# Optimization experiments

Hardware: AMD Instinct MI355X
Metric: run time of the kernel (lower is better)

Reference implementation:

```python
import jax, jax.numpy as jnp
import numpy as np

NUM_PAGES = 1024
PAGE_SIZE = 64
KV_HEADS = 8
HEAD_DIM = 128
NUM_TOKENS = 8192


def setup_inputs() -> dict:
    key = jax.random.key(0)
    k1, k2, k3 = jax.random.split(key, 3)
    kv_pages = jnp.zeros((NUM_PAGES, PAGE_SIZE, 2 * KV_HEADS, HEAD_DIM), dtype=jnp.float32)
    new_k = jax.random.normal(k1, (NUM_TOKENS, KV_HEADS, HEAD_DIM), dtype=jnp.float32)
    new_v = jax.random.normal(k2, (NUM_TOKENS, KV_HEADS, HEAD_DIM), dtype=jnp.float32)
    # distinct random destination slots (irregular but deterministic scatter);
    # mark a small tail as padding (-1) to exercise the drop path.
    dests = jax.random.permutation(k3, NUM_PAGES * PAGE_SIZE)[:NUM_TOKENS].astype(jnp.int32)
    pad = jnp.arange(NUM_TOKENS) >= (NUM_TOKENS - 128)
    token_dests = jnp.where(pad, jnp.int32(-1), dests)
    return {"kv_pages": kv_pages, "new_k": new_k, "new_v": new_v, "token_dests": token_dests}


def reference(kv_pages, new_k, new_v, token_dests):
    # kv_pages: [num_pages, page_size, 2*kv_heads, head_dim]
    # new_k/new_v: [tok, kv_heads, head_dim]; token_dests: i32[tok] flat slot index (-1 = pad)
    num_pages, page_size = kv_pages.shape[0], kv_pages.shape[1]
    kv_heads = new_k.shape[1]
    valid = token_dests >= 0
    t_pages = jnp.where(valid, token_dests // page_size, num_pages)   # OOB -> dropped
    t_slots = jnp.where(valid, token_dests % page_size, page_size)
    out = kv_pages.at[t_pages, t_slots, :kv_heads].set(new_k, mode="drop")
    out = out.at[t_pages, t_slots, kv_heads:].set(new_v, mode="drop")
    return out
```

## Files before the change

kernel.cpp:

```cpp
#include <hip/hip_runtime.h>


typedef float f4 __attribute__((ext_vector_type(4)));

__global__ void inv_init_kernel(int* __restrict__ inv, int num_slots) {
    const int stride = gridDim.x * blockDim.x;
    for (int s = blockIdx.x * blockDim.x + threadIdx.x; s < num_slots; s += stride)
        inv[s] = -1;
}

__global__ void inv_scatter_kernel(const int* __restrict__ dests, int num_tokens,
                                   int* __restrict__ inv, int num_slots) {
    const int t = blockIdx.x * blockDim.x + threadIdx.x;
    if (t >= num_tokens) return;
    const int d = dests[t];
    if (d >= 0 && d < num_slots) inv[d] = t;
}

__global__ void fused_copy_scatter(const f4* __restrict__ kv_pages,
                                   const f4* __restrict__ new_k,
                                   const f4* __restrict__ new_v,
                                   const int* __restrict__ inv,
                                   f4* __restrict__ out,
                                   int num_slots) {
    const int i = threadIdx.x;
    for (int slot = blockIdx.x; slot < num_slots; slot += gridDim.x) {
        const int t = inv[slot];
        f4* o = out + (size_t)slot * 512;
        if (t >= 0) {
            const f4* k = new_k + (size_t)t * 256;
            const f4* v = new_v + (size_t)t * 256;
            __builtin_nontemporal_store(__builtin_nontemporal_load(k + i), o + i);
            __builtin_nontemporal_store(__builtin_nontemporal_load(v + i), o + i + 256);
        } else {
            const f4* src = kv_pages + (size_t)slot * 512;
            __builtin_nontemporal_store(__builtin_nontemporal_load(src + i), o + i);
            __builtin_nontemporal_store(__builtin_nontemporal_load(src + i + 256), o + i + 256);
        }
    }
}

__global__ void kv_scatter_kernel(const f4* __restrict__ new_k,
                                  const f4* __restrict__ new_v,
                                  const int* __restrict__ dests,
                                  f4* __restrict__ out,
                                  int num_slots) {
    const int t = blockIdx.x;
    const int d = dests[t];
    if (d < 0 || d >= num_slots) return;
    const f4* k = new_k + (size_t)t * 256;
    const f4* v = new_v + (size_t)t * 256;
    f4* o = out + (size_t)d * 512;
    const int i = threadIdx.x;
    o[i]       = k[i];
    o[i + 256] = v[i];
}

extern "C" void kernel_launch(void* const* d_in, const int* in_sizes, int n_in,
                              void* d_out, int out_size, void* d_ws, size_t ws_size,
                              hipStream_t stream) {
    const float* kv_pages = (const float*)d_in[0];
    const float* new_k    = (const float*)d_in[1];
    const float* new_v    = (const float*)d_in[2];
    const int*   dests    = (const int*)d_in[3];

    const int num_tokens = in_sizes[3];
    const int row_floats = 2 * 8 * 128;
    const int num_slots  = out_size / row_floats;

    if (ws_size >= (size_t)num_slots * sizeof(int)) {
        int* inv = (int*)d_ws;
        inv_init_kernel<<<256, 256, 0, stream>>>(inv, num_slots);
        inv_scatter_kernel<<<(num_tokens + 255) / 256, 256, 0, stream>>>(
            dests, num_tokens, inv, num_slots);
        fused_copy_scatter<<<2048, 256, 0, stream>>>(
            (const f4*)kv_pages, (const f4*)new_k, (const f4*)new_v,
            inv, (f4*)d_out, num_slots);
    } else {
        hipMemcpyAsync(d_out, kv_pages, (size_t)out_size * sizeof(float),
                       hipMemcpyDeviceToDevice, stream);
        kv_scatter_kernel<<<num_tokens, 256, 0, stream>>>(
            (const f4*)new_k, (const f4*)new_v, dests, (f4*)d_out, num_slots);
    }
}
```

Before: 201.6 us.

## Map one wavefront per slot in fused copy-scatter and prefetch next inverse index

The fused copy kernel now gives each 64-lane wavefront a whole 8KB slot row, so every lane issues eight 16-byte loads and stores instead of a 256-thread block handling one row per iteration. The inverse-map entry for the next slot is loaded ahead of time so its latency overlaps the current copy. A launch-bounds hint requests occupancy of 8 blocks per CU. Together these aim to raise the number of memory operations in flight per wave and to take the dependent index load off the critical path, at the cost of more registers per thread.

```diff
diff --git a/kernel.cpp b/kernel.cpp
--- a/kernel.cpp
+++ b/kernel.cpp
@@ -17,26 +17,42 @@
     if (d >= 0 && d < num_slots) inv[d] = t;
 }
 
-__global__ void fused_copy_scatter(const f4* __restrict__ kv_pages,
-                                   const f4* __restrict__ new_k,
-                                   const f4* __restrict__ new_v,
-                                   const int* __restrict__ inv,
-                                   f4* __restrict__ out,
-                                   int num_slots) {
-    const int i = threadIdx.x;
-    for (int slot = blockIdx.x; slot < num_slots; slot += gridDim.x) {
-        const int t = inv[slot];
-        f4* o = out + (size_t)slot * 512;
+__global__ void __launch_bounds__(256, 8)
+fused_copy_scatter(const f4* __restrict__ kv_pages,
+                   const f4* __restrict__ new_k,
+                   const f4* __restrict__ new_v,
+                   const int* __restrict__ inv,
+                   f4* __restrict__ out,
+                   int num_slots) {
+    const int lane   = threadIdx.x & 63;
+    const int wave   = blockIdx.x * (blockDim.x >> 6) + (threadIdx.x >> 6);
+    const int nwaves = gridDim.x * (blockDim.x >> 6);
+
+    int slot = wave;
+    if (slot >= num_slots) return;
+    int t = inv[slot];
+
+    for (; slot < num_slots; slot += nwaves) {
+        const int nslot = slot + nwaves;
+        const int tnext = (nslot < num_slots) ? inv[nslot] : -1;
+
+        f4* o = out + (size_t)slot * 512 + lane;
         if (t >= 0) {
-            const f4* k = new_k + (size_t)t * 256;
-            const f4* v = new_v + (size_t)t * 256;
-            __builtin_nontemporal_store(__builtin_nontemporal_load(k + i), o + i);
-            __builtin_nontemporal_store(__builtin_nontemporal_load(v + i), o + i + 256);
+            const f4* k = new_k + (size_t)t * 256 + lane;
+            const f4* v = new_v + (size_t)t * 256 + lane;
+#pragma unroll
+            for (int j = 0; j < 4; ++j)
+                __builtin_nontemporal_store(__builtin_nontemporal_load(k + j * 64), o + j * 64);
+#pragma unroll
+            for (int j = 0; j < 4; ++j)
+                __builtin_nontemporal_store(__builtin_nontemporal_load(v + j * 64), o + 256 + j * 64);
         } else {
-            const f4* src = kv_pages + (size_t)slot * 512;
-            __builtin_nontemporal_store(__builtin_nontemporal_load(src + i), o + i);
-            __builtin_nontemporal_store(__builtin_nontemporal_load(src + i + 256), o + i + 256);
+            const f4* src = kv_pages + (size_t)slot * 512 + lane;
+#pragma unroll
+            for (int j = 0; j < 8; ++j)
+                __builtin_nontemporal_store(__builtin_nontemporal_load(src + j * 64), o + j * 64);
         }
+        t = tnext;
     }
 }
 
```

Result: faster. 197.1 us (-2.2%).
